# Optimization experiments

Measured on AMD Instinct MI355X. Metric: run time of the kernel, lower is better.

The kernel has to match this reference:

```python
import jax, jax.numpy as jnp
import numpy as np
from jax import lax

E, D, I, K = 8, 1024, 2048, 2
B, S = 4, 1024


def setup_inputs() -> dict:
    key = jax.random.key(0)
    k1, k2, k3, k4, k5 = jax.random.split(key, 5)
    x = jax.random.normal(k1, (B, S, D), dtype=jnp.float32)
    routing_weights = jax.random.uniform(k2, (B, S, K), dtype=jnp.float32)
    selected_experts = jax.random.randint(k3, (B, S, K), 0, E).astype(jnp.int64)
    w1 = 0.02 * jax.random.normal(k4, (E, D, I), dtype=jnp.float32)
    w2 = 0.02 * jax.random.normal(k5, (E, I, D), dtype=jnp.float32)
    return {"x": x, "routing_weights": routing_weights,
            "selected_experts": selected_experts, "w1": w1, "w2": w2}


def reference(x, routing_weights, selected_experts, w1, w2):
    shape = x.shape
    d = shape[-1]
    xf = x.reshape(-1, d)                       # [T, D]
    rw = routing_weights.reshape(xf.shape[0], -1)   # [T, K]
    se = selected_experts.reshape(xf.shape[0], -1)  # [T, K]
    n_experts = w1.shape[0]

    def body(acc, inputs):
        e, w1e, w2e = inputs
        # per-token combine weight for expert e (rw assumed >= 0; zero weight == not routed)
        wt = jnp.sum(jnp.where(se == e, rw, 0.0), axis=-1)  # [T]
        h = jax.nn.silu(xf @ w1e)                # [T, I]
        out = h @ w2e                            # [T, D]
        return acc + out * wt[:, None], None

    acc0 = jnp.zeros_like(xf)
    acc, _ = lax.scan(body, acc0, (jnp.arange(n_experts), w1, w2))
    return acc.reshape(shape)
```

## Files before the change

kernel.cpp:

```cpp
#include <hip/hip_runtime.h>
#include <stdint.h>

#define E_EXPERTS 8
#define D_DIM 1024
#define I_DIM 2048
#define T_TOKENS 4096
#define NSLOTS 8192
#define TILE 128
#define MAXPAD (NSLOTS + E_EXPERTS * TILE)
#define TPX 9

#define XCVT_BLOCKS 2048
#define PREP_GRID (1 + XCVT_BLOCKS + 4096)

typedef __attribute__((ext_vector_type(8))) short bf16x8;
typedef __attribute__((ext_vector_type(4))) float f32x4;

__device__ __forceinline__ unsigned short f2b(float f) {
  union { float f; uint32_t u; } v; v.f = f;
  uint32_t r = v.u + 0x7FFFu + ((v.u >> 16) & 1u);
  return (unsigned short)(r >> 16);
}
__device__ __forceinline__ float b2f(unsigned short u) {
  union { uint32_t u; float f; } v; v.u = ((uint32_t)u) << 16; return v.f;
}

__device__ __forceinline__ void async16(const unsigned short* g, unsigned short* l) {
  __builtin_amdgcn_global_load_lds(
      (const __attribute__((address_space(1))) void*)g,
      (__attribute__((address_space(3))) void*)l, 16, 0, 0);
}

__global__ __launch_bounds__(256) void prep_k(
    const float* __restrict__ x, const float* __restrict__ w1, const float* __restrict__ w2,
    const int* __restrict__ se,
    unsigned short* __restrict__ xb, unsigned short* __restrict__ w1t,
    unsigned short* __restrict__ w2t,
    int* __restrict__ ntiles, int* __restrict__ desc,
    int* __restrict__ tok, int* __restrict__ slot_of) {
  int b = blockIdx.x;
  int tid = threadIdx.x;

  if (b == 0) {
    __shared__ int scnt[E_EXPERTS], sbase[E_EXPERTS + 1], scur[E_EXPERTS];
    if (tid < E_EXPERTS) scnt[tid] = 0;
    __syncthreads();
    for (int s = tid; s < NSLOTS; s += 256) atomicAdd(&scnt[se[s]], 1);
    __syncthreads();
    if (tid == 0) {
      int acc = 0, nt = 0;
      for (int e = 0; e < E_EXPERTS; e++) {
        int n = scnt[e];
        sbase[e] = acc;
        scur[e] = acc;
        int pad = (n + TILE - 1) & ~(TILE - 1);
        for (int m = 0; m * TILE < pad; m++) { desc[2 * nt] = e; desc[2 * nt + 1] = acc + m * TILE; nt++; }
        acc += pad;
      }
      sbase[E_EXPERTS] = acc;
      *ntiles = nt;
    }
    __syncthreads();
    for (int e = 0; e < E_EXPERTS; e++) {
      int s0 = sbase[e] + scnt[e], s1 = sbase[e + 1];
      for (int s = s0 + tid; s < s1; s += 256) tok[s] = 0;
    }
    for (int s = tid; s < NSLOTS; s += 256) {
      int e = se[s];
      int pos = atomicAdd(&scur[e], 1);
      tok[pos] = s >> 1;
      slot_of[s] = pos;
    }
    return;
  }

  int bb = b - 1;

  if (bb < XCVT_BLOCKS) {
    size_t i = ((size_t)bb * 256 + tid) * 8;
    float4 v0 = *(const float4*)(x + i);
    float4 v1 = *(const float4*)(x + i + 4);
    ushort4 o0, o1;
    o0.x = f2b(v0.x); o0.y = f2b(v0.y); o0.z = f2b(v0.z); o0.w = f2b(v0.w);
    o1.x = f2b(v1.x); o1.y = f2b(v1.y); o1.z = f2b(v1.z); o1.w = f2b(v1.w);
    *(ushort4*)(xb + i) = o0;
    *(ushort4*)(xb + i + 4) = o1;
    return;
  }

  __shared__ float ts[64 * 129];
  int wb = bb - XCVT_BLOCKS;
  int mat = wb >> 11;
  int sub = wb & 2047;
  int e = sub >> 8, rem = sub & 255;
  const float* src; unsigned short* dst; int C, k0, n0;
  if (mat == 0) {
    int nt = rem >> 4, kt = rem & 15;
    C = I_DIM; k0 = kt * 64; n0 = nt * 128;
    src = w1 + (size_t)e * D_DIM * I_DIM;
    dst = w1t + ((size_t)((e * 16 + nt) * 16 + kt)) * 8192;
  } else {
    int nt = rem >> 5, kt = rem & 31;
    C = D_DIM; k0 = kt * 64; n0 = nt * 128;
    src = w2 + (size_t)e * D_DIM * I_DIM;
    dst = w2t + ((size_t)((e * 8 + nt) * 32 + kt)) * 8192;
  }

#pragma unroll
  for (int i = 0; i < 8; i++) {
    int f4 = i * 256 + tid;
    int row = f4 >> 5, c4 = (f4 & 31) * 4;
    float4 v = *(const float4*)(src + (size_t)(k0 + row) * C + n0 + c4);
    float* d = ts + row * 129 + c4;
    d[0] = v.x; d[1] = v.y; d[2] = v.z; d[3] = v.w;
  }
  __syncthreads();
#pragma unroll
  for (int j = 0; j < 4; j++) {
    int q = j * 256 + tid;
    int rr = q >> 3, cc8 = q & 7;
    int c = cc8 ^ (rr & 7);
    bf16x8 o;
#pragma unroll
    for (int t = 0; t < 8; t++)
      o[t] = (short)f2b(ts[(c * 8 + t) * 129 + rr]);
    *(bf16x8*)(dst + (size_t)q * 8) = o;
  }
}

template <int KLEN, int KFULL, int NDIM, int PHASE>
__global__ __launch_bounds__(256) void moe_gemm_k(
    const unsigned short* __restrict__ Amat, const unsigned short* __restrict__ Bt,
    const int* __restrict__ desc, const int* __restrict__ ntiles_p,
    const int* __restrict__ tok, unsigned short* __restrict__ Hout) {
  int id = blockIdx.x;
  int xcd = id & 7, r = id >> 3;
  int ti = xcd * TPX + r % TPX;
  int q = r / TPX;
  int nb, kh;
  if (PHASE == 1) { nb = q; kh = 0; }
  else           { kh = q & 1; nb = q >> 1; }
  if (ti >= *ntiles_p) return;
  int e = desc[2 * ti];
  int slot0 = desc[2 * ti + 1];

  __shared__ unsigned short As[128 * 64];
  __shared__ unsigned short Bs[128 * 64];

  int tid = threadIdx.x;
  int lane = tid & 63;
  int wave = tid >> 6;
  int wm = (wave >> 1) * 64, wn = (wave & 1) * 64;
  int l15 = lane & 15, quad = lane >> 4;

  f32x4 acc[4][4] = {};

  int sr = tid >> 3;
  int ldoff = (((lane & 7) ^ (lane >> 3)) * 8);

  const unsigned short* arow[4];
#pragma unroll
  for (int p = 0; p < 4; p++) {
    int rr = sr + p * 32;
    int row = (PHASE == 1) ? tok[slot0 + rr] : (slot0 + rr);
    arow[p] = Amat + (size_t)row * KFULL + kh * KLEN + ldoff;
  }
  const unsigned short* Bpack =
      Bt + ((((size_t)e * (NDIM / 128) + nb) * (KFULL / 64) + (size_t)kh * (KLEN / 64)) << 13) +
      (size_t)tid * 8;

  for (int kt = 0; kt < KLEN / 64; kt++) {
    int k0 = kt * 64;
#pragma unroll
    for (int p = 0; p < 4; p++) {
      unsigned short* adst = As + (size_t)(p * 256 + wave * 64) * 8;
      unsigned short* bdst = Bs + (size_t)(p * 256 + wave * 64) * 8;
      async16(arow[p] + k0, adst);
      async16(Bpack + (size_t)kt * 8192 + p * 2048, bdst);
    }
    __syncthreads();
#pragma unroll
    for (int ks = 0; ks < 2; ks++) {
      bf16x8 af[4], bfr[4];
#pragma unroll
      for (int i = 0; i < 4; i++) {
        int rr = wm + i * 16 + l15;
        int cc = (((ks * 4 + quad) ^ (rr & 7)) * 8);
        af[i] = *(const bf16x8*)&As[rr * 64 + cc];
      }
#pragma unroll
      for (int j = 0; j < 4; j++) {
        int rr = wn + j * 16 + l15;
        int cc = (((ks * 4 + quad) ^ (rr & 7)) * 8);
        bfr[j] = *(const bf16x8*)&Bs[rr * 64 + cc];
      }
#pragma unroll
      for (int i = 0; i < 4; i++)
#pragma unroll
        for (int j = 0; j < 4; j++)
          acc[i][j] = __builtin_amdgcn_mfma_f32_16x16x32_bf16(af[i], bfr[j], acc[i][j], 0, 0, 0);
    }
    __syncthreads();
  }

#pragma unroll
  for (int i = 0; i < 4; i++) {
    int slotr = slot0 + wm + i * 16 + quad * 4;
#pragma unroll
    for (int rg = 0; rg < 4; rg++) {
      int row = slotr + rg;
      size_t base = (PHASE == 1) ? (size_t)row * NDIM
                                 : ((size_t)kh * MAXPAD + row) * NDIM;
#pragma unroll
      for (int j = 0; j < 4; j++) {
        int col = nb * 128 + wn + j * 16 + l15;
        float v = acc[i][j][rg];
        if (PHASE == 1) v = v / (1.f + __expf(-v));
        Hout[base + col] = f2b(v);
      }
    }
  }
}

__global__ void combine_k(const unsigned short* __restrict__ y, const float* __restrict__ rw,
                          const int* __restrict__ slot_of, float* __restrict__ out) {
  int g = blockIdx.x * blockDim.x + threadIdx.x;
  int t = g >> 7, dd = (g & 127) * 8;
  int s0 = slot_of[2 * t], s1 = slot_of[2 * t + 1];
  float w0 = rw[2 * t], w1 = rw[2 * t + 1];
  const unsigned short* p00 = y + (size_t)s0 * D_DIM + dd;
  const unsigned short* p01 = y + ((size_t)MAXPAD + s0) * D_DIM + dd;
  const unsigned short* p10 = y + (size_t)s1 * D_DIM + dd;
  const unsigned short* p11 = y + ((size_t)MAXPAD + s1) * D_DIM + dd;
  ushort4 a0 = *(const ushort4*)p00, a1 = *(const ushort4*)(p00 + 4);
  ushort4 b0 = *(const ushort4*)p01, b1 = *(const ushort4*)(p01 + 4);
  ushort4 c0 = *(const ushort4*)p10, c1 = *(const ushort4*)(p10 + 4);
  ushort4 d0 = *(const ushort4*)p11, d1 = *(const ushort4*)(p11 + 4);
  float4 o0, o1;
  o0.x = w0 * (b2f(a0.x) + b2f(b0.x)) + w1 * (b2f(c0.x) + b2f(d0.x));
  o0.y = w0 * (b2f(a0.y) + b2f(b0.y)) + w1 * (b2f(c0.y) + b2f(d0.y));
  o0.z = w0 * (b2f(a0.z) + b2f(b0.z)) + w1 * (b2f(c0.z) + b2f(d0.z));
  o0.w = w0 * (b2f(a0.w) + b2f(b0.w)) + w1 * (b2f(c0.w) + b2f(d0.w));
  o1.x = w0 * (b2f(a1.x) + b2f(b1.x)) + w1 * (b2f(c1.x) + b2f(d1.x));
  o1.y = w0 * (b2f(a1.y) + b2f(b1.y)) + w1 * (b2f(c1.y) + b2f(d1.y));
  o1.z = w0 * (b2f(a1.z) + b2f(b1.z)) + w1 * (b2f(c1.z) + b2f(d1.z));
  o1.w = w0 * (b2f(a1.w) + b2f(b1.w)) + w1 * (b2f(c1.w) + b2f(d1.w));
  float* op = out + (size_t)t * D_DIM + dd;
  *(float4*)op = o0;
  *(float4*)(op + 4) = o1;
}

extern "C" void kernel_launch(void* const* d_in, const int* in_sizes, int n_in,
                              void* d_out, int out_size, void* d_ws, size_t ws_size,
                              hipStream_t stream) {
  (void)in_sizes; (void)n_in; (void)ws_size; (void)out_size;
  const float* x  = (const float*)d_in[0];
  const float* rw = (const float*)d_in[1];
  const int*   se = (const int*)d_in[2];
  const float* w1 = (const float*)d_in[3];
  const float* w2 = (const float*)d_in[4];
  float* out = (float*)d_out;
  char* ws = (char*)d_ws;

  int* ntiles  = (int*)(ws + 128);
  int* desc    = (int*)(ws + 256);
  int* tok     = (int*)(ws + 4096);
  int* slot_of = (int*)(ws + 40960);
  unsigned short* xb   = (unsigned short*)(ws + 131072);
  unsigned short* w1t  = xb + (size_t)T_TOKENS * D_DIM;
  unsigned short* w2t  = w1t + (size_t)E_EXPERTS * D_DIM * I_DIM;
  unsigned short* hbuf = w2t + (size_t)E_EXPERTS * D_DIM * I_DIM;
  unsigned short* ypart = xb;

  prep_k<<<PREP_GRID, 256, 0, stream>>>(x, w1, w2, se, xb, w1t, w2t,
                                        ntiles, desc, tok, slot_of);
  moe_gemm_k<1024, 1024, I_DIM, 1><<<8 * TPX * (I_DIM / 128), 256, 0, stream>>>(
      xb, w1t, desc, ntiles, tok, hbuf);
  moe_gemm_k<1024, 2048, D_DIM, 2><<<8 * TPX * (D_DIM / 128) * 2, 256, 0, stream>>>(
      hbuf, w2t, desc, ntiles, tok, ypart);

  combine_k<<<T_TOKENS * 128 / 256, 256, 0, stream>>>(ypart, rw, slot_of, out);
}
```

Baseline: 294.5 us.

## Load GEMM operand fragments directly from global into registers, dropping LDS staging

Removes the shared-memory tiles and barriers from the MoE GEMM kernel. Each wave now loads its A and B MFMA fragments straight from global memory into registers, double-buffered across k-steps in software. This is meant to eliminate LDS round-trips and syncthreads stalls. In exchange, the two waves sharing a row or column each fetch the same data, so global and L2 traffic goes up and the loads are less coalesced.

Result: slower. 403.0 us (+36.9%).

```diff
diff --git a/kernel.cpp b/kernel.cpp
--- a/kernel.cpp
+++ b/kernel.cpp
@@ -23,12 +23,6 @@
 }
 __device__ __forceinline__ float b2f(unsigned short u) {
   union { uint32_t u; float f; } v; v.u = ((uint32_t)u) << 16; return v.f;
-}
-
-__device__ __forceinline__ void async16(const unsigned short* g, unsigned short* l) {
-  __builtin_amdgcn_global_load_lds(
-      (const __attribute__((address_space(1))) void*)g,
-      (__attribute__((address_space(3))) void*)l, 16, 0, 0);
 }
 
 __global__ __launch_bounds__(256) void prep_k(
@@ -144,9 +138,6 @@
   int e = desc[2 * ti];
   int slot0 = desc[2 * ti + 1];
 
-  __shared__ unsigned short As[128 * 64];
-  __shared__ unsigned short Bs[128 * 64];
-
   int tid = threadIdx.x;
   int lane = tid & 63;
   int wave = tid >> 6;
@@ -155,53 +146,60 @@
 
   f32x4 acc[4][4] = {};
 
-  int sr = tid >> 3;
-  int ldoff = (((lane & 7) ^ (lane >> 3)) * 8);
-
-  const unsigned short* arow[4];
-#pragma unroll
-  for (int p = 0; p < 4; p++) {
-    int rr = sr + p * 32;
+  uint32_t aoff[4];
+#pragma unroll
+  for (int i = 0; i < 4; i++) {
+    int rr = wm + i * 16 + l15;
     int row = (PHASE == 1) ? tok[slot0 + rr] : (slot0 + rr);
-    arow[p] = Amat + (size_t)row * KFULL + kh * KLEN + ldoff;
-  }
-  const unsigned short* Bpack =
-      Bt + ((((size_t)e * (NDIM / 128) + nb) * (KFULL / 64) + (size_t)kh * (KLEN / 64)) << 13) +
-      (size_t)tid * 8;
-
-  for (int kt = 0; kt < KLEN / 64; kt++) {
-    int k0 = kt * 64;
-#pragma unroll
-    for (int p = 0; p < 4; p++) {
-      unsigned short* adst = As + (size_t)(p * 256 + wave * 64) * 8;
-      unsigned short* bdst = Bs + (size_t)(p * 256 + wave * 64) * 8;
-      async16(arow[p] + k0, adst);
-      async16(Bpack + (size_t)kt * 8192 + p * 2048, bdst);
-    }
-    __syncthreads();
-#pragma unroll
-    for (int ks = 0; ks < 2; ks++) {
-      bf16x8 af[4], bfr[4];
-#pragma unroll
-      for (int i = 0; i < 4; i++) {
-        int rr = wm + i * 16 + l15;
-        int cc = (((ks * 4 + quad) ^ (rr & 7)) * 8);
-        af[i] = *(const bf16x8*)&As[rr * 64 + cc];
-      }
-#pragma unroll
-      for (int j = 0; j < 4; j++) {
-        int rr = wn + j * 16 + l15;
-        int cc = (((ks * 4 + quad) ^ (rr & 7)) * 8);
-        bfr[j] = *(const bf16x8*)&Bs[rr * 64 + cc];
-      }
-#pragma unroll
-      for (int i = 0; i < 4; i++)
-#pragma unroll
-        for (int j = 0; j < 4; j++)
-          acc[i][j] = __builtin_amdgcn_mfma_f32_16x16x32_bf16(af[i], bfr[j], acc[i][j], 0, 0, 0);
-    }
-    __syncthreads();
-  }
+    aoff[i] = (uint32_t)row * KFULL + kh * KLEN + quad * 8;
+  }
+
+  const unsigned short* Bblock =
+      Bt + ((((size_t)e * (NDIM / 128) + nb) * (KFULL / 64) + (size_t)kh * (KLEN / 64)) << 13);
+  uint32_t boff0[4], boff1[4];
+#pragma unroll
+  for (int j = 0; j < 4; j++) {
+    int rr = wn + j * 16 + l15;
+    int p = rr & 7;
+    boff0[j] = (uint32_t)(rr * 8 + (quad ^ p)) * 8;
+    boff1[j] = (uint32_t)(rr * 8 + ((4 + quad) ^ p)) * 8;
+  }
+
+#define LOADK(AF, BF, SS, KS)                                                   \
+  do {                                                                          \
+    uint32_t kb_ = (uint32_t)(SS) * 32;                                         \
+    const unsigned short* bp_ = Bblock + ((size_t)((SS) >> 1) * 8192);          \
+    _Pragma("unroll")                                                           \
+    for (int i_ = 0; i_ < 4; i_++)                                              \
+      AF[i_] = *(const bf16x8*)(Amat + (size_t)aoff[i_] + kb_);                 \
+    _Pragma("unroll")                                                           \
+    for (int j_ = 0; j_ < 4; j_++)                                              \
+      BF[j_] = *(const bf16x8*)(bp_ + boff##KS[j_]);                            \
+  } while (0)
+
+#define MFMAS(AF, BF)                                                           \
+  do {                                                                          \
+    _Pragma("unroll")                                                           \
+    for (int i_ = 0; i_ < 4; i_++)                                              \
+      _Pragma("unroll")                                                         \
+      for (int j_ = 0; j_ < 4; j_++)                                            \
+        acc[i_][j_] =                                                           \
+            __builtin_amdgcn_mfma_f32_16x16x32_bf16(AF[i_], BF[j_],             \
+                                                    acc[i_][j_], 0, 0, 0);      \
+  } while (0)
+
+  const int NS = 2 * (KLEN / 64);
+  bf16x8 a0[4], b0[4], a1[4], b1[4];
+  LOADK(a0, b0, 0, 0);
+#pragma unroll 4
+  for (int s = 0; s < NS; s += 2) {
+    LOADK(a1, b1, s + 1, 1);
+    MFMAS(a0, b0);
+    if (s + 2 < NS) LOADK(a0, b0, s + 2, 0);
+    MFMAS(a1, b1);
+  }
+#undef LOADK
+#undef MFMAS
 
 #pragma unroll
   for (int i = 0; i < 4; i++) {
```

## Vectorize GEMM epilogue stores via swapped MFMA operands, coalesce weight-convert and combine loads

Applied to the files above, without the earlier changes.

The GEMM swaps the MFMA A/B operands so each lane holds four consecutive output columns, which lets the epilogue write ushort4 vectors instead of scalar bf16 stores. The weight-transpose kernel remaps its thread-to-element assignment for the global loads. The combine kernel now uses single 16-byte loads in place of paired 8-byte loads. Together these aim to cut store/load instruction counts and scattered memory transactions, at the cost of a different LDS write pattern in the transpose kernel.

After: 299.0 us. About the same (+1.5%).

```diff
diff --git a/kernel.cpp b/kernel.cpp
--- a/kernel.cpp
+++ b/kernel.cpp
@@ -106,10 +106,10 @@
     dst = w2t + ((size_t)((e * 8 + nt) * 32 + kt)) * 8192;
   }
 
+  int lrow = tid & 7, c4 = (tid >> 3) * 4;
 #pragma unroll
   for (int i = 0; i < 8; i++) {
-    int f4 = i * 256 + tid;
-    int row = f4 >> 5, c4 = (f4 & 31) * 4;
+    int row = i * 8 + lrow;
     float4 v = *(const float4*)(src + (size_t)(k0 + row) * C + n0 + c4);
     float* d = ts + row * 129 + c4;
     d[0] = v.x; d[1] = v.y; d[2] = v.z; d[3] = v.w;
@@ -198,26 +198,27 @@
       for (int i = 0; i < 4; i++)
 #pragma unroll
         for (int j = 0; j < 4; j++)
-          acc[i][j] = __builtin_amdgcn_mfma_f32_16x16x32_bf16(af[i], bfr[j], acc[i][j], 0, 0, 0);
+          acc[i][j] = __builtin_amdgcn_mfma_f32_16x16x32_bf16(bfr[j], af[i], acc[i][j], 0, 0, 0);
     }
     __syncthreads();
   }
 
 #pragma unroll
   for (int i = 0; i < 4; i++) {
-    int slotr = slot0 + wm + i * 16 + quad * 4;
-#pragma unroll
-    for (int rg = 0; rg < 4; rg++) {
-      int row = slotr + rg;
-      size_t base = (PHASE == 1) ? (size_t)row * NDIM
-                                 : ((size_t)kh * MAXPAD + row) * NDIM;
-#pragma unroll
-      for (int j = 0; j < 4; j++) {
-        int col = nb * 128 + wn + j * 16 + l15;
+    int slotr = slot0 + wm + i * 16 + l15;
+    size_t base = (PHASE == 1) ? (size_t)slotr * NDIM
+                               : ((size_t)kh * MAXPAD + slotr) * NDIM;
+#pragma unroll
+    for (int j = 0; j < 4; j++) {
+      int colbase = nb * 128 + wn + j * 16 + quad * 4;
+      ushort4 o;
+#pragma unroll
+      for (int rg = 0; rg < 4; rg++) {
         float v = acc[i][j][rg];
         if (PHASE == 1) v = v / (1.f + __expf(-v));
-        Hout[base + col] = f2b(v);
-      }
+        ((unsigned short*)&o)[rg] = f2b(v);
+      }
+      *(ushort4*)(Hout + base + colbase) = o;
     }
   }
 }
@@ -228,23 +229,19 @@
   int t = g >> 7, dd = (g & 127) * 8;
   int s0 = slot_of[2 * t], s1 = slot_of[2 * t + 1];
   float w0 = rw[2 * t], w1 = rw[2 * t + 1];
-  const unsigned short* p00 = y + (size_t)s0 * D_DIM + dd;
-  const unsigned short* p01 = y + ((size_t)MAXPAD + s0) * D_DIM + dd;
-  const unsigned short* p10 = y + (size_t)s1 * D_DIM + dd;
-  const unsigned short* p11 = y + ((size_t)MAXPAD + s1) * D_DIM + dd;
-  ushort4 a0 = *(const ushort4*)p00, a1 = *(const ushort4*)(p00 + 4);
-  ushort4 b0 = *(const ushort4*)p01, b1 = *(const ushort4*)(p01 + 4);
-  ushort4 c0 = *(const ushort4*)p10, c1 = *(const ushort4*)(p10 + 4);
-  ushort4 d0 = *(const ushort4*)p11, d1 = *(const ushort4*)(p11 + 4);
+  bf16x8 a = *(const bf16x8*)(y + (size_t)s0 * D_DIM + dd);
+  bf16x8 bq = *(const bf16x8*)(y + ((size_t)MAXPAD + s0) * D_DIM + dd);
+  bf16x8 c = *(const bf16x8*)(y + (size_t)s1 * D_DIM + dd);
+  bf16x8 d = *(const bf16x8*)(y + ((size_t)MAXPAD + s1) * D_DIM + dd);
   float4 o0, o1;
-  o0.x = w0 * (b2f(a0.x) + b2f(b0.x)) + w1 * (b2f(c0.x) + b2f(d0.x));
-  o0.y = w0 * (b2f(a0.y) + b2f(b0.y)) + w1 * (b2f(c0.y) + b2f(d0.y));
-  o0.z = w0 * (b2f(a0.z) + b2f(b0.z)) + w1 * (b2f(c0.z) + b2f(d0.z));
-  o0.w = w0 * (b2f(a0.w) + b2f(b0.w)) + w1 * (b2f(c0.w) + b2f(d0.w));
-  o1.x = w0 * (b2f(a1.x) + b2f(b1.x)) + w1 * (b2f(c1.x) + b2f(d1.x));
-  o1.y = w0 * (b2f(a1.y) + b2f(b1.y)) + w1 * (b2f(c1.y) + b2f(d1.y));
-  o1.z = w0 * (b2f(a1.z) + b2f(b1.z)) + w1 * (b2f(c1.z) + b2f(d1.z));
-  o1.w = w0 * (b2f(a1.w) + b2f(b1.w)) + w1 * (b2f(c1.w) + b2f(d1.w));
+  float* o = (float*)&o0;
+#pragma unroll
+  for (int k = 0; k < 8; k++) {
+    float v = w0 * (b2f((unsigned short)a[k]) + b2f((unsigned short)bq[k])) +
+              w1 * (b2f((unsigned short)c[k]) + b2f((unsigned short)d[k]));
+    if (k < 4) ((float*)&o0)[k] = v; else ((float*)&o1)[k - 4] = v;
+  }
+  (void)o;
   float* op = out + (size_t)t * D_DIM + dd;
   *(float4*)op = o0;
   *(float4*)(op + 4) = o1;
```
